# Optimization experiments

Measured on AMD Instinct MI355X. Metric: run time of the kernel, lower is better.

The kernel has to match this reference:

```python
import jax, jax.numpy as jnp
import numpy as np

C, H, O, T, B = 15, 256, 512, 60, 1024


def setup_inputs() -> dict:
    key = jax.random.key(0)
    ks = jax.random.split(key, 8)
    s = 1.0 / np.sqrt(H)
    return {
        "x": jax.random.normal(ks[0], (B, H), dtype=jnp.float32),
        "cam": jax.random.randint(ks[1], (B,), 0, C, dtype=jnp.int32),
        "W_ih": jax.random.uniform(ks[2], (C, 3 * H, H), jnp.float32, -s, s),
        "W_hh": jax.random.uniform(ks[3], (C, 3 * H, H), jnp.float32, -s, s),
        "b_ih": jax.random.uniform(ks[4], (C, 3 * H), jnp.float32, -s, s),
        "b_hh": jax.random.uniform(ks[5], (C, 3 * H), jnp.float32, -s, s),
        "Wc": jax.random.uniform(ks[6], (C, O, H), jnp.float32, -s, s),
        "bc": jax.random.uniform(ks[7], (C, O), jnp.float32, -s, s),
    }


def reference(x, cam, W_ih, W_hh, b_ih, b_hh, Wc, bc):
    # Gather per-sample (per-camera) parameters once.
    Wi = W_ih[cam]          # [B, 3H, H]
    Wh = W_hh[cam]          # [B, 3H, H]
    bi = b_ih[cam]          # [B, 3H]
    bh = b_hh[cam]          # [B, 3H]
    Wcs = Wc[cam]           # [B, O, H]
    bcs = bc[cam]           # [B, O]

    # Input is constant across timesteps -> input gate preactivations computed once.
    gi = jnp.einsum('bh,bgh->bg', x, Wi) + bi   # [B, 3H]
    gi_r, gi_z, gi_n = jnp.split(gi, 3, axis=1)

    h0 = jnp.zeros_like(x)  # [B, H]

    def step(h, _):
        gh = jnp.einsum('bh,bgh->bg', h, Wh) + bh
        gh_r, gh_z, gh_n = jnp.split(gh, 3, axis=1)
        r = jax.nn.sigmoid(gi_r + gh_r)
        z = jax.nn.sigmoid(gi_z + gh_z)
        n = jnp.tanh(gi_n + r * gh_n)
        h_new = (1.0 - z) * n + z * h
        out = jax.nn.sigmoid(jnp.einsum('bh,boh->bo', h_new, Wcs) + bcs)  # [B, O]
        return h_new, out

    _, outs = jax.lax.scan(step, h0, None, length=T)  # [T, B, O]
    return jnp.transpose(outs, (1, 2, 0))             # [B, O, T]
```

## Files before the change

### kernel.cpp

```cpp
#include <hip/hip_runtime.h>
#include <hip/hip_fp16.h>

#define C_    15
#define H_    256
#define O_    512
#define T_    60
#define B_    1024
#define G3H_  768
#define TS    16
#define MAXG  12
#define NSLOT 96
#define NU    80
#define TCH   10

typedef __attribute__((ext_vector_type(8))) short bf16x8;
typedef __attribute__((ext_vector_type(4))) float f32x4;

__device__ __forceinline__ unsigned short f2bf(float f) {
    union { float f; unsigned u; } v; v.f = f;
    return (unsigned short)((v.u + 0x7FFFu + ((v.u >> 16) & 1u)) >> 16);
}
__device__ __forceinline__ float sigf(float x) { return 1.f / (1.f + __expf(-x)); }

__global__ __launch_bounds__(256) void sort_kernel(const int* __restrict__ cam,
    int* __restrict__ order, int* __restrict__ tcam, int* __restrict__ toff,
    int* __restrict__ tcnt)
{
    __shared__ int cnt[C_], start[C_], fill[C_];
    int tid = threadIdx.x;
    if (tid < C_) cnt[tid] = 0;
    if (tid < NSLOT) { tcam[tid] = -1; toff[tid] = 0; tcnt[tid] = 0; }
    __syncthreads();
    for (int b = tid; b < B_; b += 256) atomicAdd(&cnt[cam[b]], 1);
    __syncthreads();
    if (tid == 0) {
        int run = 0;
        for (int c = 0; c < C_; ++c) { start[c] = run; fill[c] = run; run += cnt[c]; }
    }
    __syncthreads();
    for (int b = tid; b < B_; b += 256) {
        int pos = atomicAdd(&fill[cam[b]], 1);
        order[pos] = b;
    }
    __syncthreads();
    if (tid == 0) {
        int gcnt[8] = {0,0,0,0,0,0,0,0};
        for (int c = 0; c < C_; ++c) gcnt[c & 7] += (cnt[c] + TS - 1) / TS;
        int maxg = 0;
        for (int g = 0; g < 8; ++g) maxg = max(maxg, gcnt[g]);
        if (maxg <= MAXG) {
            for (int g = 0; g < 8; ++g) {
                int k = 0;
                for (int c = g; c < C_; c += 8)
                    for (int r = 0; r < cnt[c]; r += TS) {
                        int slot = g + 8 * k;
                        tcam[slot] = c; toff[slot] = start[c] + r;
                        tcnt[slot] = min(TS, cnt[c] - r); ++k;
                    }
            }
        } else {
            int ti = 0;
            for (int c = 0; c < C_; ++c)
                for (int r = 0; r < cnt[c]; r += TS) {
                    tcam[ti] = c; toff[ti] = start[c] + r;
                    tcnt[ti] = min(TS, cnt[c] - r); ++ti;
                }
        }
    }
}

__global__ __launch_bounds__(256) void cvt_kernel(const float* __restrict__ src,
    unsigned short* __restrict__ dst, int n4)
{
    int i = blockIdx.x * 256 + threadIdx.x;
    if (i < n4) {
        float4 v = ((const float4*)src)[i];
        unsigned p0 = (unsigned)f2bf(v.x) | ((unsigned)f2bf(v.y) << 16);
        unsigned p1 = (unsigned)f2bf(v.z) | ((unsigned)f2bf(v.w) << 16);
        ((uint2*)dst)[i] = make_uint2(p0, p1);
    }
}

__global__ __launch_bounds__(64) void pack_kernel(
    const float* __restrict__ Whh, const float* __restrict__ Wc,
    unsigned short* __restrict__ Wpack)
{
    int cu = blockIdx.x;
    int c = cu / NU, u = cu - c * NU;
    int lane = threadIdx.x, q = lane >> 4, l16 = lane & 15;
    const float* src = (u < 48)
        ? &Whh[((size_t)c * G3H_ + u * 16 + l16) * H_]
        : &Wc[((size_t)c * O_ + (u - 48) * 16 + l16) * H_];
    unsigned short* dst = Wpack + ((size_t)cu * 8) * 512 + lane * 8;
#pragma unroll
    for (int kk = 0; kk < 8; ++kk) {
        float4 v0 = *(const float4*)&src[kk * 32 + q * 8];
        float4 v1 = *(const float4*)&src[kk * 32 + q * 8 + 4];
        unsigned short* d = dst + kk * 512;
        d[0] = f2bf(v0.x); d[1] = f2bf(v0.y); d[2] = f2bf(v0.z); d[3] = f2bf(v0.w);
        d[4] = f2bf(v1.x); d[5] = f2bf(v1.y); d[6] = f2bf(v1.z); d[7] = f2bf(v1.w);
    }
}

__global__ __launch_bounds__(384) void gi_mfma(
    const float* __restrict__ x, const unsigned short* __restrict__ Wih_b,
    const float* __restrict__ bih, const float* __restrict__ bhh,
    const int* __restrict__ order, const int* __restrict__ tcam,
    const int* __restrict__ toff, const int* __restrict__ tcnt,
    float* __restrict__ gi)
{
    int c = tcam[blockIdx.x]; if (c < 0) return;
    int cnt = tcnt[blockIdx.x], off = toff[blockIdx.x];
    int tid = threadIdx.x;
    __shared__ unsigned short hbfs[TS * 264];
    for (int idx = tid; idx < TS * 64; idx += 384) {
        int m = idx >> 6, c4 = idx & 63;
        float4 v = make_float4(0.f, 0.f, 0.f, 0.f);
        if (m < cnt) v = *(const float4*)&x[(size_t)order[off + m] * H_ + (c4 << 2)];
        unsigned p0 = (unsigned)f2bf(v.x) | ((unsigned)f2bf(v.y) << 16);
        unsigned p1 = (unsigned)f2bf(v.z) | ((unsigned)f2bf(v.w) << 16);
        *(uint2*)&hbfs[m * 264 + (c4 << 2)] = make_uint2(p0, p1);
    }
    __syncthreads();
    int w = tid >> 6, lane = tid & 63, q = lane >> 4, l16 = lane & 15;
    f32x4 acc[2][4];
#pragma unroll
    for (int i = 0; i < 2; ++i)
#pragma unroll
        for (int nt = 0; nt < 4; ++nt) acc[i][nt] = (f32x4){0.f, 0.f, 0.f, 0.f};
    const unsigned short* bp[2];
#pragma unroll
    for (int i = 0; i < 2; ++i)
        bp[i] = Wih_b + ((size_t)c * G3H_ + (2 * w + i) * 64 + l16) * H_;
    const unsigned short* ap = &hbfs[l16 * 264 + q * 8];
#pragma unroll 2
    for (int kk = 0; kk < 8; ++kk) {
        bf16x8 a = *(const bf16x8*)(ap + kk * 32);
#pragma unroll
        for (int i = 0; i < 2; ++i)
#pragma unroll
            for (int nt = 0; nt < 4; ++nt) {
                bf16x8 b = *(const bf16x8*)(bp[i] + (size_t)nt * 16 * H_ + kk * 32 + q * 8);
                acc[i][nt] = __builtin_amdgcn_mfma_f32_16x16x32_bf16(a, b, acc[i][nt], 0, 0, 0);
            }
    }
#pragma unroll
    for (int i = 0; i < 2; ++i) {
        int u = 2 * w + i;
#pragma unroll
        for (int nt = 0; nt < 4; ++nt) {
            int col = u * 64 + nt * 16 + l16;
            float bias = bih[c * G3H_ + col] + (col < 2 * H_ ? bhh[c * G3H_ + col] : 0.f);
#pragma unroll
            for (int r = 0; r < 4; ++r) {
                int m = q * 4 + r;
                gi[((size_t)(blockIdx.x * TS + m)) * G3H_ + col] = acc[i][nt][r] + bias;
            }
        }
    }
}

__global__ __launch_bounds__(512, 2) void persist_kernel(
    const unsigned short* __restrict__ Wpack, const float* __restrict__ bhh,
    const float* __restrict__ gi, const int* __restrict__ tcam,
    unsigned short* __restrict__ htraj)
{
    int slot = blockIdx.x;
    int c = tcam[slot]; if (c < 0) return;
    int tid = threadIdx.x, w = tid >> 6, lane = tid & 63, q = lane >> 4, l16 = lane & 15;

    __shared__ float gisT[G3H_][20];
    __shared__ unsigned short hbf[2][16][264];

    for (int idx = tid; idx < TS * G3H_; idx += 512) {
        int m = idx / G3H_, col = idx - m * G3H_;
        gisT[col][m] = gi[((size_t)(slot * TS + m)) * G3H_ + col];
    }

    bf16x8 wf[6][8];
#pragma unroll
    for (int ii = 0; ii < 3; ++ii)
#pragma unroll
        for (int jj = 0; jj < 2; ++jj)
#pragma unroll
            for (int kk = 0; kk < 8; ++kk)
                wf[ii * 2 + jj][kk] = *(const bf16x8*)(
                    Wpack + (((size_t)(c * NU + ii * 16 + w + 8 * jj)) * 8 + kk) * 512 + lane * 8);

    float bhn[2], hreg[2][4];
#pragma unroll
    for (int i = 0; i < 2; ++i) {
        int col = (w + 8 * i) * 16 + l16;
        bhn[i] = bhh[c * G3H_ + 2 * H_ + col];
#pragma unroll
        for (int r = 0; r < 4; ++r) hreg[i][r] = 0.f;
    }
    unsigned short* hp = htraj + ((size_t)slot * TS + q * 4) * 256 + w * 16 + l16;
    __syncthreads();

#pragma unroll 2
    for (int s = 0; s < T_; ++s) {
        int wbuf = s & 1, rbuf = wbuf ^ 1;
        f32x4 acc[6];
#pragma unroll
        for (int ui = 0; ui < 6; ++ui) acc[ui] = (f32x4){0.f, 0.f, 0.f, 0.f};
        if (s > 0) {
#pragma unroll
            for (int kk = 0; kk < 8; ++kk) {
                bf16x8 a = *(const bf16x8*)&hbf[rbuf][l16][kk * 32 + q * 8];
#pragma unroll
                for (int ui = 0; ui < 6; ++ui)
                    acc[ui] = __builtin_amdgcn_mfma_f32_16x16x32_bf16(a, wf[ui][kk], acc[ui], 0, 0, 0);
            }
        }
#pragma unroll
        for (int i = 0; i < 2; ++i) {
            int col = (w + 8 * i) * 16 + l16;
            f32x4 gr = *(const f32x4*)&gisT[col][q * 4];
            f32x4 gz = *(const f32x4*)&gisT[H_ + col][q * 4];
            f32x4 gn = *(const f32x4*)&gisT[2 * H_ + col][q * 4];
#pragma unroll
            for (int r = 0; r < 4; ++r) {
                float rr = sigf(gr[r] + acc[i][r]);
                float zz = sigf(gz[r] + acc[2 + i][r]);
                float pre = gn[r] + rr * (acc[4 + i][r] + bhn[i]);
                float nn = 2.f * sigf(2.f * pre) - 1.f;
                float hn = (1.f - zz) * nn + zz * hreg[i][r];
                hreg[i][r] = hn;
                unsigned short hb = f2bf(hn);
                hbf[wbuf][q * 4 + r][col] = hb;
                hp[r * 256 + i * 128] = hb;
            }
        }
        hp += (size_t)NSLOT * TS * 256;
        asm volatile("s_waitcnt lgkmcnt(0)" ::: "memory");
        __builtin_amdgcn_s_barrier();
        __builtin_amdgcn_sched_barrier(0);
    }
}

__global__ __launch_bounds__(512, 2) void out_kernel(
    const unsigned short* __restrict__ Wpack, const float* __restrict__ bc,
    const unsigned short* __restrict__ htraj, const int* __restrict__ order,
    const int* __restrict__ tcam, const int* __restrict__ toff,
    const int* __restrict__ tcnt, unsigned short* __restrict__ outT,
    int direct, float* __restrict__ outp)
{
    int slot = blockIdx.x;
    int c = tcam[slot]; if (c < 0) return;
    int n = tcnt[slot], off = toff[slot];
    int tid = threadIdx.x, w = tid >> 6, lane = tid & 63, q = lane >> 4, l16 = lane & 15;
    __shared__ unsigned short hb[2][16][264];
    __shared__ int ord16[16];
    if (tid < 16) ord16[tid] = (tid < n) ? order[off + tid] : -1;

    bf16x8 wf[4][8];
    const unsigned short* wb = Wpack + ((size_t)c * NU + 48 + w * 4) * 8 * 512 + lane * 8;
#pragma unroll
    for (int ui = 0; ui < 4; ++ui)
#pragma unroll
        for (int kk = 0; kk < 8; ++kk)
            wf[ui][kk] = *(const bf16x8*)(wb + ((size_t)ui * 8 + kk) * 512);
    float bcr[4];
#pragma unroll
    for (int ui = 0; ui < 4; ++ui)
        bcr[ui] = bc[c * O_ + (w * 4 + ui) * 16 + l16];

    int m = tid >> 5, c8 = (tid & 31) * 8;
    const unsigned short* hsrc =
        &htraj[(((size_t)(blockIdx.y * TCH) * NSLOT + slot) * 16 + m) * 256 + c8];
    uint4 stg = *(const uint4*)hsrc;
    *(uint4*)&hb[0][m][c8] = stg;
    __syncthreads();

    for (int ti = 0; ti < TCH; ++ti) {
        int t = blockIdx.y * TCH + ti;
        int cur = ti & 1;
        if (ti + 1 < TCH)
            stg = *(const uint4*)(hsrc + (size_t)(ti + 1) * NSLOT * TS * 256);
        f32x4 acc[4];
#pragma unroll
        for (int ui = 0; ui < 4; ++ui) acc[ui] = (f32x4){0.f, 0.f, 0.f, 0.f};
#pragma unroll
        for (int kk = 0; kk < 8; ++kk) {
            bf16x8 a = *(const bf16x8*)&hb[cur][l16][kk * 32 + q * 8];
#pragma unroll
            for (int ui = 0; ui < 4; ++ui)
                acc[ui] = __builtin_amdgcn_mfma_f32_16x16x32_bf16(a, wf[ui][kk], acc[ui], 0, 0, 0);
        }
#pragma unroll
        for (int ui = 0; ui < 4; ++ui) {
            int o = (w * 4 + ui) * 16 + l16;
#pragma unroll
            for (int r = 0; r < 4; ++r) {
                int b = ord16[q * 4 + r];
                if (b >= 0) {
                    float val = sigf(acc[ui][r] + bcr[ui]);
                    if (direct) outp[((size_t)b * O_ + o) * T_ + t] = val;
                    else outT[((size_t)t * B_ + b) * O_ + o] =
                             __half_as_ushort(__float2half_rn(val));
                }
            }
        }
        if (ti + 1 < TCH) {
            *(uint4*)&hb[cur ^ 1][m][c8] = stg;
            asm volatile("s_waitcnt lgkmcnt(0)" ::: "memory");
            __builtin_amdgcn_s_barrier();
            __builtin_amdgcn_sched_barrier(0);
        }
    }
}

__global__ __launch_bounds__(256) void transpose_kernel(
    const unsigned short* __restrict__ outT, float* __restrict__ outp)
{
    int b = blockIdx.x, o0 = blockIdx.y * 64;
    __shared__ float ts[T_][65];
    int tid = threadIdx.x;
    for (int idx = tid; idx < T_ * 64; idx += 256) {
        int t = idx >> 6, o = idx & 63;
        ts[t][o] = __half2float(__ushort_as_half(outT[((size_t)t * B_ + b) * O_ + o0 + o]));
    }
    __syncthreads();
    for (int idx = tid; idx < 64 * T_; idx += 256) {
        int o = idx / T_, t = idx - o * T_;
        outp[((size_t)b * O_ + o0 + o) * T_ + t] = ts[t][o];
    }
}

extern "C" void kernel_launch(void* const* d_in, const int* in_sizes, int n_in,
                              void* d_out, int out_size, void* d_ws, size_t ws_size,
                              hipStream_t stream)
{
    const float* x   = (const float*)d_in[0];
    const int*   cam = (const int*)d_in[1];
    const float* Wih = (const float*)d_in[2];
    const float* Whh = (const float*)d_in[3];
    const float* bih = (const float*)d_in[4];
    const float* bhh = (const float*)d_in[5];
    const float* Wc  = (const float*)d_in[6];
    const float* bc  = (const float*)d_in[7];
    float* outp = (float*)d_out;

    char* w = (char*)d_ws;
    unsigned short* Wih_b = (unsigned short*)w; w += (size_t)C_ * G3H_ * H_ * 2;
    unsigned short* Wpack = (unsigned short*)w; w += (size_t)C_ * NU * 8 * 512 * 2;
    int* order = (int*)w; w += B_ * 4;
    int* tcam  = (int*)w; w += NSLOT * 4;
    int* toff  = (int*)w; w += NSLOT * 4;
    int* tcnt  = (int*)w; w += NSLOT * 4;
    float* gi  = (float*)w; w += (size_t)NSLOT * TS * G3H_ * 4;
    unsigned short* htraj = (unsigned short*)w; w += (size_t)T_ * NSLOT * 16 * 256 * 2;
    unsigned short* outT = (unsigned short*)w;
    size_t need = (size_t)(w - (char*)d_ws) + (size_t)T_ * B_ * O_ * 2;
    int direct = (ws_size < need) ? 1 : 0;

    sort_kernel<<<1, 256, 0, stream>>>(cam, order, tcam, toff, tcnt);
    cvt_kernel<<<(C_ * G3H_ * H_ / 4 + 255) / 256, 256, 0, stream>>>(Wih, Wih_b, C_ * G3H_ * H_ / 4);
    pack_kernel<<<C_ * NU, 64, 0, stream>>>(Whh, Wc, Wpack);
    gi_mfma<<<NSLOT, 384, 0, stream>>>(x, Wih_b, bih, bhh, order, tcam, toff, tcnt, gi);
    persist_kernel<<<NSLOT, 512, 0, stream>>>(Wpack, bhh, gi, tcam, htraj);
    out_kernel<<<dim3(NSLOT, T_ / TCH), 512, 0, stream>>>(Wpack, bc, htraj, order, tcam,
                                                          toff, tcnt, outT, direct, outp);
    if (!direct)
        transpose_kernel<<<dim3(B_, O_ / 64), 256, 0, stream>>>(outT, outp);
}
```

Measured before the change: 439.9 us.

## Fuse prep kernels, register-resident gi in recurrence, drop transpose via direct strided output

Sort, Wih bf16 conversion and weight packing now run in a single launch, with block ranges dispatching to each task. The persistent GRU kernel drops the shared-memory gi tile and keeps gi in registers, seeding the MFMA accumulators with gi and the bias so there are fewer adds and no initial barrier. The output kernel is split across a larger grid, with one 16-column tile per wave and 10 timesteps per block. Each block writes its 10 consecutive timesteps straight into the final [B,O,T] layout as float2 stores, removing the half-precision staging buffer and the separate transpose kernel. The trade-offs are more registers in the recurrence, which now runs at occupancy 1, and each out_kernel block reloading its weights and h trajectory.

After: 491.5 us. 11.7% more time.

```diff
diff --git a/kernel.cpp b/kernel.cpp
--- a/kernel.cpp
+++ b/kernel.cpp
@@ -11,7 +11,8 @@
 #define MAXG  12
 #define NSLOT 96
 #define NU    80
-#define TCH   10
+#define PACKB 300
+#define CVTB  2880
 
 typedef __attribute__((ext_vector_type(8))) short bf16x8;
 typedef __attribute__((ext_vector_type(4))) float f32x4;
@@ -22,83 +23,77 @@
 }
 __device__ __forceinline__ float sigf(float x) { return 1.f / (1.f + __expf(-x)); }
 
-__global__ __launch_bounds__(256) void sort_kernel(const int* __restrict__ cam,
+__global__ __launch_bounds__(256) void prep_kernel(
+    const int* __restrict__ cam, const float* __restrict__ Wih,
+    const float* __restrict__ Whh, const float* __restrict__ Wc,
     int* __restrict__ order, int* __restrict__ tcam, int* __restrict__ toff,
-    int* __restrict__ tcnt)
-{
-    __shared__ int cnt[C_], start[C_], fill[C_];
-    int tid = threadIdx.x;
-    if (tid < C_) cnt[tid] = 0;
-    if (tid < NSLOT) { tcam[tid] = -1; toff[tid] = 0; tcnt[tid] = 0; }
-    __syncthreads();
-    for (int b = tid; b < B_; b += 256) atomicAdd(&cnt[cam[b]], 1);
-    __syncthreads();
-    if (tid == 0) {
-        int run = 0;
-        for (int c = 0; c < C_; ++c) { start[c] = run; fill[c] = run; run += cnt[c]; }
-    }
-    __syncthreads();
-    for (int b = tid; b < B_; b += 256) {
-        int pos = atomicAdd(&fill[cam[b]], 1);
-        order[pos] = b;
-    }
-    __syncthreads();
-    if (tid == 0) {
-        int gcnt[8] = {0,0,0,0,0,0,0,0};
-        for (int c = 0; c < C_; ++c) gcnt[c & 7] += (cnt[c] + TS - 1) / TS;
-        int maxg = 0;
-        for (int g = 0; g < 8; ++g) maxg = max(maxg, gcnt[g]);
-        if (maxg <= MAXG) {
-            for (int g = 0; g < 8; ++g) {
-                int k = 0;
-                for (int c = g; c < C_; c += 8)
+    int* __restrict__ tcnt, unsigned short* __restrict__ Wih_b,
+    unsigned short* __restrict__ Wpack)
+{
+    int bid = blockIdx.x, tid = threadIdx.x;
+    if (bid == 0) {
+        __shared__ int cnt[C_], start[C_], fill[C_];
+        if (tid < C_) cnt[tid] = 0;
+        if (tid < NSLOT) { tcam[tid] = -1; toff[tid] = 0; tcnt[tid] = 0; }
+        __syncthreads();
+        for (int b = tid; b < B_; b += 256) atomicAdd(&cnt[cam[b]], 1);
+        __syncthreads();
+        if (tid == 0) {
+            int run = 0;
+            for (int c = 0; c < C_; ++c) { start[c] = run; fill[c] = run; run += cnt[c]; }
+        }
+        __syncthreads();
+        for (int b = tid; b < B_; b += 256) {
+            int pos = atomicAdd(&fill[cam[b]], 1);
+            order[pos] = b;
+        }
+        __syncthreads();
+        if (tid == 0) {
+            int gcnt[8] = {0,0,0,0,0,0,0,0};
+            for (int c = 0; c < C_; ++c) gcnt[c & 7] += (cnt[c] + TS - 1) / TS;
+            int maxg = 0;
+            for (int g = 0; g < 8; ++g) maxg = max(maxg, gcnt[g]);
+            if (maxg <= MAXG) {
+                for (int g = 0; g < 8; ++g) {
+                    int k = 0;
+                    for (int c = g; c < C_; c += 8)
+                        for (int r = 0; r < cnt[c]; r += TS) {
+                            int slot = g + 8 * k;
+                            tcam[slot] = c; toff[slot] = start[c] + r;
+                            tcnt[slot] = min(TS, cnt[c] - r); ++k;
+                        }
+                }
+            } else {
+                int ti = 0;
+                for (int c = 0; c < C_; ++c)
                     for (int r = 0; r < cnt[c]; r += TS) {
-                        int slot = g + 8 * k;
-                        tcam[slot] = c; toff[slot] = start[c] + r;
-                        tcnt[slot] = min(TS, cnt[c] - r); ++k;
+                        tcam[ti] = c; toff[ti] = start[c] + r;
+                        tcnt[ti] = min(TS, cnt[c] - r); ++ti;
                     }
             }
-        } else {
-            int ti = 0;
-            for (int c = 0; c < C_; ++c)
-                for (int r = 0; r < cnt[c]; r += TS) {
-                    tcam[ti] = c; toff[ti] = start[c] + r;
-                    tcnt[ti] = min(TS, cnt[c] - r); ++ti;
-                }
-        }
-    }
-}
-
-__global__ __launch_bounds__(256) void cvt_kernel(const float* __restrict__ src,
-    unsigned short* __restrict__ dst, int n4)
-{
-    int i = blockIdx.x * 256 + threadIdx.x;
-    if (i < n4) {
-        float4 v = ((const float4*)src)[i];
+        }
+    } else if (bid <= PACKB) {
+        int cu = (bid - 1) * 4 + (tid >> 6);
+        int c = cu / NU, u = cu - c * NU;
+        int lane = tid & 63, q = lane >> 4, l16 = lane & 15;
+        const float* src = (u < 48)
+            ? &Whh[((size_t)c * G3H_ + u * 16 + l16) * H_]
+            : &Wc[((size_t)c * O_ + (u - 48) * 16 + l16) * H_];
+        unsigned short* dst = Wpack + ((size_t)cu * 8) * 512 + lane * 8;
+#pragma unroll
+        for (int kk = 0; kk < 8; ++kk) {
+            float4 v0 = *(const float4*)&src[kk * 32 + q * 8];
+            float4 v1 = *(const float4*)&src[kk * 32 + q * 8 + 4];
+            unsigned short* d = dst + kk * 512;
+            d[0] = f2bf(v0.x); d[1] = f2bf(v0.y); d[2] = f2bf(v0.z); d[3] = f2bf(v0.w);
+            d[4] = f2bf(v1.x); d[5] = f2bf(v1.y); d[6] = f2bf(v1.z); d[7] = f2bf(v1.w);
+        }
+    } else {
+        int i = (bid - 1 - PACKB) * 256 + tid;
+        float4 v = ((const float4*)Wih)[i];
         unsigned p0 = (unsigned)f2bf(v.x) | ((unsigned)f2bf(v.y) << 16);
         unsigned p1 = (unsigned)f2bf(v.z) | ((unsigned)f2bf(v.w) << 16);
-        ((uint2*)dst)[i] = make_uint2(p0, p1);
-    }
-}
-
-__global__ __launch_bounds__(64) void pack_kernel(
-    const float* __restrict__ Whh, const float* __restrict__ Wc,
-    unsigned short* __restrict__ Wpack)
-{
-    int cu = blockIdx.x;
-    int c = cu / NU, u = cu - c * NU;
-    int lane = threadIdx.x, q = lane >> 4, l16 = lane & 15;
-    const float* src = (u < 48)
-        ? &Whh[((size_t)c * G3H_ + u * 16 + l16) * H_]
-        : &Wc[((size_t)c * O_ + (u - 48) * 16 + l16) * H_];
-    unsigned short* dst = Wpack + ((size_t)cu * 8) * 512 + lane * 8;
-#pragma unroll
-    for (int kk = 0; kk < 8; ++kk) {
-        float4 v0 = *(const float4*)&src[kk * 32 + q * 8];
-        float4 v1 = *(const float4*)&src[kk * 32 + q * 8 + 4];
-        unsigned short* d = dst + kk * 512;
-        d[0] = f2bf(v0.x); d[1] = f2bf(v0.y); d[2] = f2bf(v0.z); d[3] = f2bf(v0.w);
-        d[4] = f2bf(v1.x); d[5] = f2bf(v1.y); d[6] = f2bf(v1.z); d[7] = f2bf(v1.w);
+        ((uint2*)Wih_b)[i] = make_uint2(p0, p1);
     }
 }
 
@@ -160,7 +155,7 @@
     }
 }
 
-__global__ __launch_bounds__(512, 2) void persist_kernel(
+__global__ __launch_bounds__(512, 1) void persist_kernel(
     const unsigned short* __restrict__ Wpack, const float* __restrict__ bhh,
     const float* __restrict__ gi, const int* __restrict__ tcam,
     unsigned short* __restrict__ htraj)
@@ -169,13 +164,7 @@
     int c = tcam[slot]; if (c < 0) return;
     int tid = threadIdx.x, w = tid >> 6, lane = tid & 63, q = lane >> 4, l16 = lane & 15;
 
-    __shared__ float gisT[G3H_][20];
     __shared__ unsigned short hbf[2][16][264];
-
-    for (int idx = tid; idx < TS * G3H_; idx += 512) {
-        int m = idx / G3H_, col = idx - m * G3H_;
-        gisT[col][m] = gi[((size_t)(slot * TS + m)) * G3H_ + col];
-    }
 
     bf16x8 wf[6][8];
 #pragma unroll
@@ -187,23 +176,34 @@
                 wf[ii * 2 + jj][kk] = *(const bf16x8*)(
                     Wpack + (((size_t)(c * NU + ii * 16 + w + 8 * jj)) * 8 + kk) * 512 + lane * 8);
 
-    float bhn[2], hreg[2][4];
+    float gir[2][4], giz[2][4], gin[2][4], bhn[2], hreg[2][4];
 #pragma unroll
     for (int i = 0; i < 2; ++i) {
         int col = (w + 8 * i) * 16 + l16;
         bhn[i] = bhh[c * G3H_ + 2 * H_ + col];
 #pragma unroll
-        for (int r = 0; r < 4; ++r) hreg[i][r] = 0.f;
+        for (int r = 0; r < 4; ++r) {
+            size_t row = (size_t)(slot * TS + q * 4 + r) * G3H_;
+            gir[i][r] = gi[row + col];
+            giz[i][r] = gi[row + H_ + col];
+            gin[i][r] = gi[row + 2 * H_ + col];
+            hreg[i][r] = 0.f;
+        }
     }
     unsigned short* hp = htraj + ((size_t)slot * TS + q * 4) * 256 + w * 16 + l16;
-    __syncthreads();
 
 #pragma unroll 2
     for (int s = 0; s < T_; ++s) {
         int wbuf = s & 1, rbuf = wbuf ^ 1;
         f32x4 acc[6];
 #pragma unroll
-        for (int ui = 0; ui < 6; ++ui) acc[ui] = (f32x4){0.f, 0.f, 0.f, 0.f};
+        for (int i = 0; i < 2; ++i)
+#pragma unroll
+            for (int r = 0; r < 4; ++r) {
+                acc[i][r] = gir[i][r];
+                acc[2 + i][r] = giz[i][r];
+                acc[4 + i][r] = bhn[i];
+            }
         if (s > 0) {
 #pragma unroll
             for (int kk = 0; kk < 8; ++kk) {
@@ -216,14 +216,11 @@
 #pragma unroll
         for (int i = 0; i < 2; ++i) {
             int col = (w + 8 * i) * 16 + l16;
-            f32x4 gr = *(const f32x4*)&gisT[col][q * 4];
-            f32x4 gz = *(const f32x4*)&gisT[H_ + col][q * 4];
-            f32x4 gn = *(const f32x4*)&gisT[2 * H_ + col][q * 4];
 #pragma unroll
             for (int r = 0; r < 4; ++r) {
-                float rr = sigf(gr[r] + acc[i][r]);
-                float zz = sigf(gz[r] + acc[2 + i][r]);
-                float pre = gn[r] + rr * (acc[4 + i][r] + bhn[i]);
+                float rr = sigf(acc[i][r]);
+                float zz = sigf(acc[2 + i][r]);
+                float pre = gin[i][r] + rr * acc[4 + i][r];
                 float nn = 2.f * sigf(2.f * pre) - 1.f;
                 float hn = (1.f - zz) * nn + zz * hreg[i][r];
                 hreg[i][r] = hn;
@@ -243,88 +240,62 @@
     const unsigned short* __restrict__ Wpack, const float* __restrict__ bc,
     const unsigned short* __restrict__ htraj, const int* __restrict__ order,
     const int* __restrict__ tcam, const int* __restrict__ toff,
-    const int* __restrict__ tcnt, unsigned short* __restrict__ outT,
-    int direct, float* __restrict__ outp)
+    const int* __restrict__ tcnt, float* __restrict__ outp)
 {
     int slot = blockIdx.x;
     int c = tcam[slot]; if (c < 0) return;
     int n = tcnt[slot], off = toff[slot];
+    int tz = blockIdx.z;
     int tid = threadIdx.x, w = tid >> 6, lane = tid & 63, q = lane >> 4, l16 = lane & 15;
     __shared__ unsigned short hb[2][16][264];
     __shared__ int ord16[16];
     if (tid < 16) ord16[tid] = (tid < n) ? order[off + tid] : -1;
 
-    bf16x8 wf[4][8];
-    const unsigned short* wb = Wpack + ((size_t)c * NU + 48 + w * 4) * 8 * 512 + lane * 8;
-#pragma unroll
-    for (int ui = 0; ui < 4; ++ui)
-#pragma unroll
-        for (int kk = 0; kk < 8; ++kk)
-            wf[ui][kk] = *(const bf16x8*)(wb + ((size_t)ui * 8 + kk) * 512);
-    float bcr[4];
-#pragma unroll
-    for (int ui = 0; ui < 4; ++ui)
-        bcr[ui] = bc[c * O_ + (w * 4 + ui) * 16 + l16];
+    int u = blockIdx.y * 8 + w;
+    bf16x8 wf[8];
+    const unsigned short* wb = Wpack + ((size_t)c * NU + 48 + u) * 8 * 512 + lane * 8;
+#pragma unroll
+    for (int kk = 0; kk < 8; ++kk) wf[kk] = *(const bf16x8*)(wb + (size_t)kk * 512);
+    float bcr = bc[c * O_ + u * 16 + l16];
 
     int m = tid >> 5, c8 = (tid & 31) * 8;
     const unsigned short* hsrc =
-        &htraj[(((size_t)(blockIdx.y * TCH) * NSLOT + slot) * 16 + m) * 256 + c8];
+        &htraj[(((size_t)(tz * 10) * NSLOT + slot) * 16 + m) * 256 + c8];
     uint4 stg = *(const uint4*)hsrc;
     *(uint4*)&hb[0][m][c8] = stg;
     __syncthreads();
 
-    for (int ti = 0; ti < TCH; ++ti) {
-        int t = blockIdx.y * TCH + ti;
+    float vals[4][10];
+#pragma unroll
+    for (int ti = 0; ti < 10; ++ti) {
         int cur = ti & 1;
-        if (ti + 1 < TCH)
+        if (ti + 1 < 10)
             stg = *(const uint4*)(hsrc + (size_t)(ti + 1) * NSLOT * TS * 256);
-        f32x4 acc[4];
-#pragma unroll
-        for (int ui = 0; ui < 4; ++ui) acc[ui] = (f32x4){0.f, 0.f, 0.f, 0.f};
+        f32x4 acc = (f32x4){0.f, 0.f, 0.f, 0.f};
 #pragma unroll
         for (int kk = 0; kk < 8; ++kk) {
             bf16x8 a = *(const bf16x8*)&hb[cur][l16][kk * 32 + q * 8];
-#pragma unroll
-            for (int ui = 0; ui < 4; ++ui)
-                acc[ui] = __builtin_amdgcn_mfma_f32_16x16x32_bf16(a, wf[ui][kk], acc[ui], 0, 0, 0);
-        }
-#pragma unroll
-        for (int ui = 0; ui < 4; ++ui) {
-            int o = (w * 4 + ui) * 16 + l16;
-#pragma unroll
-            for (int r = 0; r < 4; ++r) {
-                int b = ord16[q * 4 + r];
-                if (b >= 0) {
-                    float val = sigf(acc[ui][r] + bcr[ui]);
-                    if (direct) outp[((size_t)b * O_ + o) * T_ + t] = val;
-                    else outT[((size_t)t * B_ + b) * O_ + o] =
-                             __half_as_ushort(__float2half_rn(val));
-                }
-            }
-        }
-        if (ti + 1 < TCH) {
+            acc = __builtin_amdgcn_mfma_f32_16x16x32_bf16(a, wf[kk], acc, 0, 0, 0);
+        }
+#pragma unroll
+        for (int r = 0; r < 4; ++r) vals[r][ti] = sigf(acc[r] + bcr);
+        if (ti + 1 < 10) {
             *(uint4*)&hb[cur ^ 1][m][c8] = stg;
             asm volatile("s_waitcnt lgkmcnt(0)" ::: "memory");
             __builtin_amdgcn_s_barrier();
             __builtin_amdgcn_sched_barrier(0);
         }
     }
-}
-
-__global__ __launch_bounds__(256) void transpose_kernel(
-    const unsigned short* __restrict__ outT, float* __restrict__ outp)
-{
-    int b = blockIdx.x, o0 = blockIdx.y * 64;
-    __shared__ float ts[T_][65];
-    int tid = threadIdx.x;
-    for (int idx = tid; idx < T_ * 64; idx += 256) {
-        int t = idx >> 6, o = idx & 63;
-        ts[t][o] = __half2float(__ushort_as_half(outT[((size_t)t * B_ + b) * O_ + o0 + o]));
-    }
-    __syncthreads();
-    for (int idx = tid; idx < 64 * T_; idx += 256) {
-        int o = idx / T_, t = idx - o * T_;
-        outp[((size_t)b * O_ + o0 + o) * T_ + t] = ts[t][o];
+    int o = u * 16 + l16;
+#pragma unroll
+    for (int r = 0; r < 4; ++r) {
+        int b = ord16[q * 4 + r];
+        if (b >= 0) {
+            float* dst = &outp[((size_t)b * O_ + o) * T_ + tz * 10];
+#pragma unroll
+            for (int j = 0; j < 5; ++j)
+                *(float2*)&dst[j * 2] = make_float2(vals[r][2 * j], vals[r][2 * j + 1]);
+        }
     }
 }
 
@@ -350,18 +321,12 @@
     int* toff  = (int*)w; w += NSLOT * 4;
     int* tcnt  = (int*)w; w += NSLOT * 4;
     float* gi  = (float*)w; w += (size_t)NSLOT * TS * G3H_ * 4;
-    unsigned short* htraj = (unsigned short*)w; w += (size_t)T_ * NSLOT * 16 * 256 * 2;
-    unsigned short* outT = (unsigned short*)w;
-    size_t need = (size_t)(w - (char*)d_ws) + (size_t)T_ * B_ * O_ * 2;
-    int direct = (ws_size < need) ? 1 : 0;
-
-    sort_kernel<<<1, 256, 0, stream>>>(cam, order, tcam, toff, tcnt);
-    cvt_kernel<<<(C_ * G3H_ * H_ / 4 + 255) / 256, 256, 0, stream>>>(Wih, Wih_b, C_ * G3H_ * H_ / 4);
-    pack_kernel<<<C_ * NU, 64, 0, stream>>>(Whh, Wc, Wpack);
+    unsigned short* htraj = (unsigned short*)w;
+
+    prep_kernel<<<1 + PACKB + CVTB, 256, 0, stream>>>(cam, Wih, Whh, Wc, order, tcam,
+                                                      toff, tcnt, Wih_b, Wpack);
     gi_mfma<<<NSLOT, 384, 0, stream>>>(x, Wih_b, bih, bhh, order, tcam, toff, tcnt, gi);
     persist_kernel<<<NSLOT, 512, 0, stream>>>(Wpack, bhh, gi, tcam, htraj);
-    out_kernel<<<dim3(NSLOT, T_ / TCH), 512, 0, stream>>>(Wpack, bc, htraj, order, tcam,
-                                                          toff, tcnt, outT, direct, outp);
-    if (!direct)
-        transpose_kernel<<<dim3(B_, O_ / 64), 256, 0, stream>>>(outT, outp);
-}
+    out_kernel<<<dim3(NSLOT, 4, 6), 512, 0, stream>>>(Wpack, bc, htraj, order, tcam,
+                                                      toff, tcnt, outp);
+}
```
